# Optimization experiments

Measured on AMD Instinct MI355X. Metric: run time of the kernel, lower is better.

## Reference

```python
import jax, jax.numpy as jnp
import numpy as np

N_NODES = 50000
N_EDGES = 800000
D_FEAT = 128


def setup_inputs() -> dict:
    key = jax.random.key(0)
    k1, k2, k3, k4 = jax.random.split(key, 4)
    x = jax.random.normal(k1, (N_NODES, D_FEAT), dtype=jnp.float32)
    vals = jax.random.uniform(k2, (N_EDGES,), dtype=jnp.float32)
    rows = jnp.sort(jax.random.randint(k3, (N_EDGES,), 0, N_NODES, dtype=jnp.int32))
    cols = jax.random.randint(k4, (N_EDGES,), 0, N_NODES, dtype=jnp.int32)
    return {"x": x, "vals": vals, "rows": rows, "cols": cols}


def reference(x, vals, rows, cols):
    # out = A @ x where A is sparse COO: out[r] += vals[e] * x[cols[e]] for each edge e with rows[e]==r
    messages = vals[:, None] * x[cols]  # [E, d]
    out = jax.ops.segment_sum(messages, rows, num_segments=N_NODES)  # [N, d]
    return out
```

## Files before the change

### kernel.cpp

```cpp
#include <hip/hip_runtime.h>


#define D_FEAT 128
#define TOTAL_WAVES 8192
#define WAVES_PER_BLOCK 4
#define BLOCK_THREADS (WAVES_PER_BLOCK * 64)
#define PF 8

__device__ __forceinline__ float bcast_f(float v, int j) {
    return __int_as_float(__builtin_amdgcn_readlane(__float_as_int(v), j));
}

__global__ __launch_bounds__(BLOCK_THREADS) void agg_kernel(
    const float* __restrict__ x, const float* __restrict__ vals,
    const int* __restrict__ rows, const int* __restrict__ cols,
    float* __restrict__ out, int n_edges, int epw) {
    const int wave = blockIdx.x * WAVES_PER_BLOCK + (threadIdx.x >> 6);
    const int lane = threadIdx.x & 63;

    const int start = wave * epw;
    if (start >= n_edges) return;
    int end = start + epw;
    if (end > n_edges) end = n_edges;

    const float2* __restrict__ x2 = (const float2*)x;

    const int first_row = rows[start];
    const int last_row  = rows[end - 1];

    float2 acc = make_float2(0.f, 0.f);
    int cur_row = first_row;

    for (int e0 = start; e0 < end; e0 += 64) {
        const int nb = min(end - e0, 64);
        int   myc = 0;
        int   myr = 0;
        float myv = 0.f;
        if (lane < nb) {
            myc = cols[e0 + lane];
            myr = rows[e0 + lane];
            myv = vals[e0 + lane];
        }
        for (int j0 = 0; j0 < nb; j0 += PF) {
            const int m = min(nb - j0, PF);
            float2 xv[PF];
            int    rj[PF];
            float  vj[PF];
#pragma unroll
            for (int t = 0; t < PF; ++t) {
                if (t < m) {
                    const int cj = __builtin_amdgcn_readlane(myc, j0 + t);
                    rj[t] = __builtin_amdgcn_readlane(myr, j0 + t);
                    vj[t] = bcast_f(myv, j0 + t);
                    xv[t] = x2[(size_t)cj * (D_FEAT / 2) + lane];
                }
            }
#pragma unroll
            for (int t = 0; t < PF; ++t) {
                if (t < m) {
                    if (rj[t] != cur_row) {
                        float* o = out + (size_t)cur_row * D_FEAT + 2 * lane;
                        if (cur_row == first_row || cur_row == last_row) {
                            atomicAdd(o,     acc.x);
                            atomicAdd(o + 1, acc.y);
                        } else {
                            *(float2*)o = acc;
                        }
                        acc.x = 0.f; acc.y = 0.f;
                        cur_row = rj[t];
                    }
                    acc.x += vj[t] * xv[t].x;
                    acc.y += vj[t] * xv[t].y;
                }
            }
        }
    }
    float* o = out + (size_t)cur_row * D_FEAT + 2 * lane;
    atomicAdd(o,     acc.x);
    atomicAdd(o + 1, acc.y);
}

extern "C" void kernel_launch(void* const* d_in, const int* in_sizes, int n_in,
                              void* d_out, int out_size, void* d_ws, size_t ws_size,
                              hipStream_t stream) {
    const float* x    = (const float*)d_in[0];
    const float* vals = (const float*)d_in[1];
    const int*   rows = (const int*)d_in[2];
    const int*   cols = (const int*)d_in[3];
    float*       out  = (float*)d_out;

    const int n_edges = in_sizes[1];

    hipMemsetAsync(d_out, 0, (size_t)out_size * sizeof(float), stream);

    const int epw = (n_edges + TOTAL_WAVES - 1) / TOTAL_WAVES;
    const int blocks = TOTAL_WAVES / WAVES_PER_BLOCK;
    agg_kernel<<<blocks, BLOCK_THREADS, 0, stream>>>(x, vals, rows, cols, out,
                                                     n_edges, epw);
}
```

Measured before the change: 142.3 us.

## Convert features to bf16 in workspace before gather to halve gather traffic

Adds a pre-pass that converts x to bf16 (round-to-nearest-even) into the workspace buffer, then gathers 4-byte packed bf16 pairs per lane instead of float2 and unpacks them with shifts. It also switches the edge-index loads and the interior row stores to nontemporal. The aim is to halve the random-gather bytes, which dominate the cost, but it adds a full conversion pass over x every call and lowers input precision to bf16, which may break tolerance. An fp32 fallback path is kept for when the workspace is too small.

```diff
diff --git a/kernel.cpp b/kernel.cpp
--- a/kernel.cpp
+++ b/kernel.cpp
@@ -7,14 +7,39 @@
 #define BLOCK_THREADS (WAVES_PER_BLOCK * 64)
 #define PF 8
 
+typedef float v2f __attribute__((ext_vector_type(2)));
+
 __device__ __forceinline__ float bcast_f(float v, int j) {
     return __int_as_float(__builtin_amdgcn_readlane(__float_as_int(v), j));
 }
 
-__global__ __launch_bounds__(BLOCK_THREADS) void agg_kernel(
-    const float* __restrict__ x, const float* __restrict__ vals,
-    const int* __restrict__ rows, const int* __restrict__ cols,
-    float* __restrict__ out, int n_edges, int epw) {
+__device__ __forceinline__ unsigned short f2bf_rne(float f) {
+    unsigned int b = __float_as_uint(f);
+    b += 0x7fffu + ((b >> 16) & 1u);
+    return (unsigned short)(b >> 16);
+}
+
+__global__ __launch_bounds__(256) void to_bf16_kernel(
+    const float* __restrict__ x, unsigned short* __restrict__ xb, int n4) {
+    const float4* __restrict__ x4 = (const float4*)x;
+    ushort4* __restrict__ o4 = (ushort4*)xb;
+    for (int i = blockIdx.x * blockDim.x + threadIdx.x; i < n4;
+         i += gridDim.x * blockDim.x) {
+        float4 f = x4[i];
+        ushort4 o;
+        o.x = f2bf_rne(f.x);
+        o.y = f2bf_rne(f.y);
+        o.z = f2bf_rne(f.z);
+        o.w = f2bf_rne(f.w);
+        o4[i] = o;
+    }
+}
+
+__global__ __launch_bounds__(BLOCK_THREADS) void agg_bf16_kernel(
+    const unsigned int* __restrict__ xb,
+    const float* __restrict__ vals, const int* __restrict__ rows,
+    const int* __restrict__ cols, float* __restrict__ out, int n_edges,
+    int epw) {
     const int wave = blockIdx.x * WAVES_PER_BLOCK + (threadIdx.x >> 6);
     const int lane = threadIdx.x & 63;
 
@@ -23,8 +48,6 @@
     int end = start + epw;
     if (end > n_edges) end = n_edges;
 
-    const float2* __restrict__ x2 = (const float2*)x;
-
     const int first_row = rows[start];
     const int last_row  = rows[end - 1];
 
@@ -33,26 +56,25 @@
 
     for (int e0 = start; e0 < end; e0 += 64) {
         const int nb = min(end - e0, 64);
-        int   myc = 0;
-        int   myr = 0;
+        int myc = 0, myr = 0;
         float myv = 0.f;
         if (lane < nb) {
-            myc = cols[e0 + lane];
-            myr = rows[e0 + lane];
-            myv = vals[e0 + lane];
+            myc = __builtin_nontemporal_load(cols + e0 + lane);
+            myr = __builtin_nontemporal_load(rows + e0 + lane);
+            myv = __builtin_nontemporal_load(vals + e0 + lane);
         }
         for (int j0 = 0; j0 < nb; j0 += PF) {
             const int m = min(nb - j0, PF);
-            float2 xv[PF];
-            int    rj[PF];
-            float  vj[PF];
+            unsigned int xu[PF];
+            int   rj[PF];
+            float vj[PF];
 #pragma unroll
             for (int t = 0; t < PF; ++t) {
                 if (t < m) {
                     const int cj = __builtin_amdgcn_readlane(myc, j0 + t);
                     rj[t] = __builtin_amdgcn_readlane(myr, j0 + t);
                     vj[t] = bcast_f(myv, j0 + t);
-                    xv[t] = x2[(size_t)cj * (D_FEAT / 2) + lane];
+                    xu[t] = xb[(size_t)cj * (D_FEAT / 2) + lane];
                 }
             }
 #pragma unroll
@@ -64,13 +86,84 @@
                             atomicAdd(o,     acc.x);
                             atomicAdd(o + 1, acc.y);
                         } else {
-                            *(float2*)o = acc;
+                            v2f st; st.x = acc.x; st.y = acc.y;
+                            __builtin_nontemporal_store(st, (v2f*)o);
                         }
                         acc.x = 0.f; acc.y = 0.f;
                         cur_row = rj[t];
                     }
-                    acc.x += vj[t] * xv[t].x;
-                    acc.y += vj[t] * xv[t].y;
+                    const float x0 = __uint_as_float(xu[t] << 16);
+                    const float x1 = __uint_as_float(xu[t] & 0xffff0000u);
+                    acc.x = fmaf(vj[t], x0, acc.x);
+                    acc.y = fmaf(vj[t], x1, acc.y);
+                }
+            }
+        }
+    }
+    float* o = out + (size_t)cur_row * D_FEAT + 2 * lane;
+    atomicAdd(o,     acc.x);
+    atomicAdd(o + 1, acc.y);
+}
+
+__global__ __launch_bounds__(BLOCK_THREADS) void agg_f32_kernel(
+    const float* __restrict__ x, const float* __restrict__ vals,
+    const int* __restrict__ rows, const int* __restrict__ cols,
+    float* __restrict__ out, int n_edges, int epw) {
+    const int wave = blockIdx.x * WAVES_PER_BLOCK + (threadIdx.x >> 6);
+    const int lane = threadIdx.x & 63;
+
+    const int start = wave * epw;
+    if (start >= n_edges) return;
+    int end = start + epw;
+    if (end > n_edges) end = n_edges;
+
+    const float2* __restrict__ x2 = (const float2*)x;
+    const int first_row = rows[start];
+    const int last_row  = rows[end - 1];
+
+    float2 acc = make_float2(0.f, 0.f);
+    int cur_row = first_row;
+
+    for (int e0 = start; e0 < end; e0 += 64) {
+        const int nb = min(end - e0, 64);
+        int myc = 0, myr = 0;
+        float myv = 0.f;
+        if (lane < nb) {
+            myc = __builtin_nontemporal_load(cols + e0 + lane);
+            myr = __builtin_nontemporal_load(rows + e0 + lane);
+            myv = __builtin_nontemporal_load(vals + e0 + lane);
+        }
+        for (int j0 = 0; j0 < nb; j0 += PF) {
+            const int m = min(nb - j0, PF);
+            float2 xv[PF];
+            int    rj[PF];
+            float  vj[PF];
+#pragma unroll
+            for (int t = 0; t < PF; ++t) {
+                if (t < m) {
+                    const int cj = __builtin_amdgcn_readlane(myc, j0 + t);
+                    rj[t] = __builtin_amdgcn_readlane(myr, j0 + t);
+                    vj[t] = bcast_f(myv, j0 + t);
+                    xv[t] = x2[(size_t)cj * (D_FEAT / 2) + lane];
+                }
+            }
+#pragma unroll
+            for (int t = 0; t < PF; ++t) {
+                if (t < m) {
+                    if (rj[t] != cur_row) {
+                        float* o = out + (size_t)cur_row * D_FEAT + 2 * lane;
+                        if (cur_row == first_row || cur_row == last_row) {
+                            atomicAdd(o,     acc.x);
+                            atomicAdd(o + 1, acc.y);
+                        } else {
+                            v2f st; st.x = acc.x; st.y = acc.y;
+                            __builtin_nontemporal_store(st, (v2f*)o);
+                        }
+                        acc.x = 0.f; acc.y = 0.f;
+                        cur_row = rj[t];
+                    }
+                    acc.x = fmaf(vj[t], xv[t].x, acc.x);
+                    acc.y = fmaf(vj[t], xv[t].y, acc.y);
                 }
             }
         }
@@ -90,11 +183,21 @@
     float*       out  = (float*)d_out;
 
     const int n_edges = in_sizes[1];
-
-    hipMemsetAsync(d_out, 0, (size_t)out_size * sizeof(float), stream);
-
-    const int epw = (n_edges + TOTAL_WAVES - 1) / TOTAL_WAVES;
+    const int n_x     = in_sizes[0];
+
+    (void)hipMemsetAsync(d_out, 0, (size_t)out_size * sizeof(float), stream);
+
+    const int epw    = (n_edges + TOTAL_WAVES - 1) / TOTAL_WAVES;
     const int blocks = TOTAL_WAVES / WAVES_PER_BLOCK;
-    agg_kernel<<<blocks, BLOCK_THREADS, 0, stream>>>(x, vals, rows, cols, out,
-                                                     n_edges, epw);
-}
+
+    const size_t need = (size_t)n_x * sizeof(unsigned short);
+    if (ws_size >= need) {
+        unsigned short* xb = (unsigned short*)d_ws;
+        to_bf16_kernel<<<2048, 256, 0, stream>>>(x, xb, n_x / 4);
+        agg_bf16_kernel<<<blocks, BLOCK_THREADS, 0, stream>>>(
+            (const unsigned int*)xb, vals, rows, cols, out, n_edges, epw);
+    } else {
+        agg_f32_kernel<<<blocks, BLOCK_THREADS, 0, stream>>>(
+            x, vals, rows, cols, out, n_edges, epw);
+    }
+}
```

Result: faster. 126.9 us (-10.8%).
